# Kernel optimization log

Hardware: AMD Instinct MI355X
Metric: run time of the kernel (lower is better)

Reference implementation:

```python
import jax, jax.numpy as jnp
import numpy as np


def _upsample_axis(V, axis):
    """Double size along `axis` by linear interp at half-integer coords with edge clamp.
    out[..., 2i, ...] = V[i]; out[..., 2i+1, ...] = 0.5*(V[i] + V[min(i+1, n-1)])
    This is exactly the SpatialTransformer linear sampling of V at locations f/2.
    """
    n = V.shape[axis]
    last = jax.lax.slice_in_dim(V, n - 1, n, axis=axis)  # clamped edge neighbor
    nxt = jnp.concatenate([jax.lax.slice_in_dim(V, 1, n, axis=axis), last], axis=axis)
    mid = 0.5 * (V + nxt)
    out = jnp.stack([V, mid], axis=axis + 1)  # interleave even/odd samples
    shape = list(V.shape)
    shape[axis] = 2 * n
    return out.reshape(shape)


def setup_inputs() -> dict:
    key = jax.random.key(0)
    V = jax.random.normal(key, (1, 80, 96, 112, 16), dtype=jnp.float32)
    return {"V": V}


def reference(V):
    # V: [B, D1..Dn, C] channels-last volume; upsample every spatial axis by 2
    # via multilinear interpolation (separable since sample coords are axis-aligned
    # half-integers f/2, matching interp_upsampling's identity-grid + (-f/2) offset).
    out = V
    for ax in range(1, V.ndim - 1):
        out = _upsample_axis(out, ax)
    return out
```

## Files before the change

kernel.cpp:

```cpp
#include <hip/hip_runtime.h>


#define DV 80
#define HV 96
#define WV 112

__device__ __forceinline__ float4 avg4(float4 x, float4 y) {
    return make_float4(0.5f * (x.x + y.x), 0.5f * (x.y + y.y),
                       0.5f * (x.z + y.z), 0.5f * (x.w + y.w));
}

__global__ __launch_bounds__(448) void UpsampleInterp_kernel(
        const float4* __restrict__ in, float4* __restrict__ out) {
    const int ho  = blockIdx.x;
    const int dof = blockIdx.y;
    const int tx  = threadIdx.x;
    const int c4  = tx & 3;
    const int wi  = tx >> 2;

    const int d0  = dof >> 1;
    const int h0  = ho >> 1;
    const int wib = (wi + 1 < WV) ? wi + 1 : WV - 1;

    const int rowstride = WV * 4;
    const int base00 = (d0 * HV + h0) * rowstride + c4;

    const bool dodd = dof & 1;
    const bool hodd = ho & 1;

    float4 a, b;
    if (!dodd && !hodd) {
        a = in[base00 + wi * 4];
        b = in[base00 + wib * 4];
    } else if (!dodd) {
        const int h1 = (h0 + 1 < HV) ? h0 + 1 : HV - 1;
        const int base01 = (d0 * HV + h1) * rowstride + c4;
        a = avg4(in[base00 + wi * 4],  in[base01 + wi * 4]);
        b = avg4(in[base00 + wib * 4], in[base01 + wib * 4]);
    } else if (!hodd) {
        const int d1 = (d0 + 1 < DV) ? d0 + 1 : DV - 1;
        const int base10 = (d1 * HV + h0) * rowstride + c4;
        a = avg4(in[base00 + wi * 4],  in[base10 + wi * 4]);
        b = avg4(in[base00 + wib * 4], in[base10 + wib * 4]);
    } else {
        const int d1 = (d0 + 1 < DV) ? d0 + 1 : DV - 1;
        const int h1 = (h0 + 1 < HV) ? h0 + 1 : HV - 1;
        const int base01 = (d0 * HV + h1) * rowstride + c4;
        const int base10 = (d1 * HV + h0) * rowstride + c4;
        const int base11 = (d1 * HV + h1) * rowstride + c4;
        a = avg4(avg4(in[base00 + wi * 4],  in[base10 + wi * 4]),
                 avg4(in[base01 + wi * 4],  in[base11 + wi * 4]));
        b = avg4(avg4(in[base00 + wib * 4], in[base10 + wib * 4]),
                 avg4(in[base01 + wib * 4], in[base11 + wib * 4]));
    }

    const int obase = (dof * (2 * HV) + ho) * (2 * WV * 4) + c4;
    out[obase + (2 * wi) * 4]     = a;
    out[obase + (2 * wi + 1) * 4] = avg4(a, b);
}

extern "C" void kernel_launch(void* const* d_in, const int* in_sizes, int n_in,
                              void* d_out, int out_size, void* d_ws, size_t ws_size,
                              hipStream_t stream) {
    const float4* in = (const float4*)d_in[0];
    float4* out = (float4*)d_out;
    dim3 grid(2 * HV, 2 * DV);
    UpsampleInterp_kernel<<<grid, 448, 0, stream>>>(in, out);
}
```

Measured before the change: 493.6 us.

## Compute 2x2 output rows per block from one input row-quad with full-width threads

Each block now handles one input (d0,h0) position and writes all four output rows (even/odd in d and h), loading the four neighbouring input rows once and reusing them. Each thread now owns one output float4 column, so stores are contiguous per thread index and the even/odd w split moves into the thread mapping. This removes the branchy per-row case selection and lets the four output rows share loads instead of reloading them across separate blocks. In exchange each thread issues eight loads and four stores, and blocks grow to 896 threads, which may lower occupancy flexibility.

Result: faster. 478.3 us (-3.1%).

```diff
diff --git a/kernel.cpp b/kernel.cpp
--- a/kernel.cpp
+++ b/kernel.cpp
@@ -4,59 +4,53 @@
 #define DV 80
 #define HV 96
 #define WV 112
+#define ROW4 (WV * 4)
+#define OROW4 (2 * WV * 4)
 
 __device__ __forceinline__ float4 avg4(float4 x, float4 y) {
     return make_float4(0.5f * (x.x + y.x), 0.5f * (x.y + y.y),
                        0.5f * (x.z + y.z), 0.5f * (x.w + y.w));
 }
 
-__global__ __launch_bounds__(448) void UpsampleInterp_kernel(
+__global__ __launch_bounds__(896) void UpsampleInterp_kernel(
         const float4* __restrict__ in, float4* __restrict__ out) {
-    const int ho  = blockIdx.x;
-    const int dof = blockIdx.y;
-    const int tx  = threadIdx.x;
-    const int c4  = tx & 3;
-    const int wi  = tx >> 2;
+    const int h0 = blockIdx.x;
+    const int d0 = blockIdx.y;
+    const int t  = threadIdx.x;
+    const int c4 = t & 3;
+    const int wo = t >> 2;
+    const int wi = wo >> 1;
+    const int wodd = wo & 1;
+    const int wib = (wi + 1 < WV) ? wi + 1 : WV - 1;
+    const int i1 = wodd ? wib : wi;
 
-    const int d0  = dof >> 1;
-    const int h0  = ho >> 1;
-    const int wib = (wi + 1 < WV) ? wi + 1 : WV - 1;
+    const int d1 = (d0 + 1 < DV) ? d0 + 1 : DV - 1;
+    const int h1 = (h0 + 1 < HV) ? h0 + 1 : HV - 1;
 
-    const int rowstride = WV * 4;
-    const int base00 = (d0 * HV + h0) * rowstride + c4;
+    const int baseA = (d0 * HV + h0) * ROW4 + c4;
+    const int baseB = (d0 * HV + h1) * ROW4 + c4;
+    const int baseC = (d1 * HV + h0) * ROW4 + c4;
+    const int baseD = (d1 * HV + h1) * ROW4 + c4;
 
-    const bool dodd = dof & 1;
-    const bool hodd = ho & 1;
+    const float4 A0 = in[baseA + 4 * wi], A1 = in[baseA + 4 * i1];
+    const float4 B0 = in[baseB + 4 * wi], B1 = in[baseB + 4 * i1];
+    const float4 C0 = in[baseC + 4 * wi], C1 = in[baseC + 4 * i1];
+    const float4 D0 = in[baseD + 4 * wi], D1 = in[baseD + 4 * i1];
 
-    float4 a, b;
-    if (!dodd && !hodd) {
-        a = in[base00 + wi * 4];
-        b = in[base00 + wib * 4];
-    } else if (!dodd) {
-        const int h1 = (h0 + 1 < HV) ? h0 + 1 : HV - 1;
-        const int base01 = (d0 * HV + h1) * rowstride + c4;
-        a = avg4(in[base00 + wi * 4],  in[base01 + wi * 4]);
-        b = avg4(in[base00 + wib * 4], in[base01 + wib * 4]);
-    } else if (!hodd) {
-        const int d1 = (d0 + 1 < DV) ? d0 + 1 : DV - 1;
-        const int base10 = (d1 * HV + h0) * rowstride + c4;
-        a = avg4(in[base00 + wi * 4],  in[base10 + wi * 4]);
-        b = avg4(in[base00 + wib * 4], in[base10 + wib * 4]);
-    } else {
-        const int d1 = (d0 + 1 < DV) ? d0 + 1 : DV - 1;
-        const int h1 = (h0 + 1 < HV) ? h0 + 1 : HV - 1;
-        const int base01 = (d0 * HV + h1) * rowstride + c4;
-        const int base10 = (d1 * HV + h0) * rowstride + c4;
-        const int base11 = (d1 * HV + h1) * rowstride + c4;
-        a = avg4(avg4(in[base00 + wi * 4],  in[base10 + wi * 4]),
-                 avg4(in[base01 + wi * 4],  in[base11 + wi * 4]));
-        b = avg4(avg4(in[base00 + wib * 4], in[base10 + wib * 4]),
-                 avg4(in[base01 + wib * 4], in[base11 + wib * 4]));
-    }
+    const float4 ab0 = avg4(A0, B0), ab1 = avg4(A1, B1);
+    const float4 ac0 = avg4(A0, C0), ac1 = avg4(A1, C1);
+    const float4 bd0 = avg4(B0, D0), bd1 = avg4(B1, D1);
 
-    const int obase = (dof * (2 * HV) + ho) * (2 * WV * 4) + c4;
-    out[obase + (2 * wi) * 4]     = a;
-    out[obase + (2 * wi + 1) * 4] = avg4(a, b);
+    const float4 r00 = avg4(A0, A1);
+    const float4 r01 = avg4(ab0, ab1);
+    const float4 r10 = avg4(ac0, ac1);
+    const float4 r11 = avg4(avg4(ac0, bd0), avg4(ac1, bd1));
+
+    const int ob = ((2 * d0) * (2 * HV) + (2 * h0)) * OROW4 + t;
+    out[ob]                     = r00;
+    out[ob + OROW4]             = r01;
+    out[ob + (2 * HV) * OROW4]          = r10;
+    out[ob + (2 * HV) * OROW4 + OROW4]  = r11;
 }
 
 extern "C" void kernel_launch(void* const* d_in, const int* in_sizes, int n_in,
@@ -64,6 +58,6 @@
                               hipStream_t stream) {
     const float4* in = (const float4*)d_in[0];
     float4* out = (float4*)d_out;
-    dim3 grid(2 * HV, 2 * DV);
-    UpsampleInterp_kernel<<<grid, 448, 0, stream>>>(in, out);
+    dim3 grid(HV, DV);
+    UpsampleInterp_kernel<<<grid, 896, 0, stream>>>(in, out);
 }
```
